# Optimization experiments

Measured on AMD Instinct MI355X. Metric: run time of the kernel, lower is better.

## Reference

```python
import jax, jax.numpy as jnp
import numpy as np

IN_FEATURES = 4096
OUT_FEATURES = 11008
GROUP_SIZE = 128
N_HIGH = 1024   # int(0.25*4096)//8*8
N_LOW = 3072    # (4096-1024)//8*8
M_TOKENS = 64


def unpack_6bit(packed, original_k):
    # packed: [K*3//4, N] uint8 values stored as int32
    _, N = packed.shape
    p = packed.reshape(original_k // 4, 3, N)
    b0, b1, b2 = p[:, 0], p[:, 1], p[:, 2]
    v0 = b0 & 63
    v1 = ((b0 >> 6) & 3) | ((b1 & 15) << 2)
    v2 = ((b1 >> 4) & 15) | ((b2 & 3) << 4)
    v3 = (b2 >> 2) & 63
    return jnp.stack([v0, v1, v2, v3], axis=1).reshape(original_k, N)


def unpack_5bit(packed, original_k):
    # packed: [K*5//8, N]
    _, N = packed.shape
    p = packed.reshape(original_k // 8, 5, N)
    b = [p[:, i] for i in range(5)]
    v0 = b[0] & 31
    v1 = ((b[0] >> 5) & 7) | ((b[1] & 3) << 3)
    v2 = (b[1] >> 2) & 31
    v3 = ((b[1] >> 7) & 1) | ((b[2] & 15) << 1)
    v4 = ((b[2] >> 4) & 15) | ((b[3] & 1) << 4)
    v5 = (b[3] >> 1) & 31
    v6 = ((b[3] >> 6) & 3) | ((b[4] & 7) << 2)
    v7 = (b[4] >> 3) & 31
    return jnp.stack([v0, v1, v2, v3, v4, v5, v6, v7], axis=1).reshape(original_k, N)


def dequant_region(W_q, scales, half_range):
    # W_q: [K, N] ints in [0, 2*half_range]; scales: [num_groups, N]
    K, N = W_q.shape
    G = scales.shape[0]
    Wg = (W_q.astype(jnp.float32) - float(half_range)).reshape(G, GROUP_SIZE, N)
    return (Wg * scales[:, None, :]).reshape(K, N)


def setup_inputs() -> dict:
    key = jax.random.key(0)
    ks = jax.random.split(key, 7)
    x = jax.random.normal(ks[0], (M_TOKENS, IN_FEATURES), dtype=jnp.float32)
    W_high_packed = jax.random.randint(ks[1], (N_HIGH * 3 // 4, OUT_FEATURES), 0, 256, dtype=jnp.int32)
    W_low_packed = jax.random.randint(ks[2], (N_LOW * 5 // 8, OUT_FEATURES), 0, 256, dtype=jnp.int32)
    scales_high = jax.random.uniform(ks[3], (N_HIGH // GROUP_SIZE, OUT_FEATURES), dtype=jnp.float32) * 0.02 + 1e-4
    scales_low = jax.random.uniform(ks[4], (N_LOW // GROUP_SIZE, OUT_FEATURES), dtype=jnp.float32) * 0.02 + 1e-4
    col_indices = jax.random.permutation(ks[5], IN_FEATURES).astype(jnp.int32)
    bias = jax.random.normal(ks[6], (OUT_FEATURES,), dtype=jnp.float32) * 0.02
    return {"x": x, "W_high_packed": W_high_packed, "W_low_packed": W_low_packed,
            "scales_high": scales_high, "scales_low": scales_low,
            "col_indices": col_indices, "bias": bias}


def reference(x, W_high_packed, W_low_packed, scales_high, scales_low, col_indices, bias):
    # Unpack mixed 6-bit / 5-bit weights and group-dequantize.
    Wq_high = unpack_6bit(W_high_packed, N_HIGH)          # [1024, N], 0..63
    Wq_low = unpack_5bit(W_low_packed, N_LOW)             # [3072, N], 0..31
    W_high = dequant_region(Wq_high, scales_high, 31)     # 6-bit half_range = 31
    W_low = dequant_region(Wq_low, scales_low, 15)        # 5-bit half_range = 15
    # Column-sensitivity reorder of activations, then split high/low regions.
    x_perm = x[:, col_indices]                            # [M, K]
    x_high = x_perm[:, :N_HIGH]
    x_low = x_perm[:, N_HIGH:N_HIGH + N_LOW]
    out = x_high @ W_high + x_low @ W_low + bias          # [M, N]
    return out
```

## Files before the change

kernel.cpp:

```cpp
#include <hip/hip_runtime.h>


#define NFEAT 11008
#define KTOT  4096

typedef _Float16 half8 __attribute__((ext_vector_type(8)));
typedef float    f32x4 __attribute__((ext_vector_type(4)));

__global__ __launch_bounds__(256) void prep_xfrag(const float* __restrict__ x,
                                                  const int* __restrict__ col,
                                                  _Float16* __restrict__ xfrag) {
    int idx = blockIdx.x * 256 + threadIdx.x;
    int j  = idx & 7;
    int l  = (idx >> 3) & 63;
    int mt = (idx >> 9) & 3;
    int s  = idx >> 11;
    int k  = s * 32 + ((l >> 4) << 3) + j;
    int m  = mt * 16 + (l & 15);
    xfrag[idx] = (_Float16)x[m * KTOT + col[k]];
}

__global__ __launch_bounds__(256, 4) void gemm_kernel(const int* __restrict__ Wh,
                                                      const int* __restrict__ Wl,
                                                      const float* __restrict__ sh,
                                                      const float* __restrict__ sl,
                                                      const _Float16* __restrict__ xfrag,
                                                      float* __restrict__ dst,
                                                      int atomic_mode) {
    const int n0   = blockIdx.x * 64;
    const int kc   = blockIdx.y;
    const int klen = KTOT / gridDim.y;
    const int k0   = kc * klen;
    const int lane = threadIdx.x & 63;
    const int wave = threadIdx.x >> 6;

    const int n  = n0 + wave * 16 + (lane & 15);
    const int kb = (lane >> 4) << 3;

    f32x4 acc[4];
#pragma unroll
    for (int i = 0; i < 4; ++i) acc[i] = (f32x4){0.f, 0.f, 0.f, 0.f};

    const int ngroups = klen >> 7;

    if (k0 < 1024) {
        for (int g = 0; g < ngroups; ++g) {
            const float s    = sh[((k0 >> 7) + g) * NFEAT + n];
            const float moff = -31.0f * s;
#pragma unroll
            for (int st = 0; st < 4; ++st) {
                const int k = k0 + g * 128 + st * 32 + kb;
                const int G = k >> 2;
                const int* bp = Wh + 3 * G * NFEAT + n;
                const int b0 = bp[0];         const int b1 = bp[NFEAT];
                const int b2 = bp[2 * NFEAT]; const int b3 = bp[3 * NFEAT];
                const int b4 = bp[4 * NFEAT]; const int b5 = bp[5 * NFEAT];
                int v0 = b0 & 63;
                int v1 = ((b0 >> 6) & 3) | ((b1 & 15) << 2);
                int v2 = ((b1 >> 4) & 15) | ((b2 & 3) << 4);
                int v3 = (b2 >> 2) & 63;
                int v4 = b3 & 63;
                int v5 = ((b3 >> 6) & 3) | ((b4 & 15) << 2);
                int v6 = ((b4 >> 4) & 15) | ((b5 & 3) << 4);
                int v7 = (b5 >> 2) & 63;
                half8 b;
                b[0] = (_Float16)fmaf((float)v0, s, moff);
                b[1] = (_Float16)fmaf((float)v1, s, moff);
                b[2] = (_Float16)fmaf((float)v2, s, moff);
                b[3] = (_Float16)fmaf((float)v3, s, moff);
                b[4] = (_Float16)fmaf((float)v4, s, moff);
                b[5] = (_Float16)fmaf((float)v5, s, moff);
                b[6] = (_Float16)fmaf((float)v6, s, moff);
                b[7] = (_Float16)fmaf((float)v7, s, moff);
                const int sg = (k0 >> 5) + g * 4 + st;
#pragma unroll
                for (int mt = 0; mt < 4; ++mt) {
                    half8 a = *(const half8*)(xfrag + (((sg * 4 + mt) * 64 + lane) << 3));
                    acc[mt] = __builtin_amdgcn_mfma_f32_16x16x32_f16(a, b, acc[mt], 0, 0, 0);
                }
            }
        }
    } else {
        const int kl0 = k0 - 1024;
        for (int g = 0; g < ngroups; ++g) {
            const float s    = sl[((kl0 >> 7) + g) * NFEAT + n];
            const float moff = -15.0f * s;
#pragma unroll
            for (int st = 0; st < 4; ++st) {
                const int kl = kl0 + g * 128 + st * 32 + kb;
                const int G8 = kl >> 3;
                const int* bp = Wl + 5 * G8 * NFEAT + n;
                const int b0 = bp[0];         const int b1 = bp[NFEAT];
                const int b2 = bp[2 * NFEAT]; const int b3 = bp[3 * NFEAT];
                const int b4 = bp[4 * NFEAT];
                int v0 = b0 & 31;
                int v1 = ((b0 >> 5) & 7) | ((b1 & 3) << 3);
                int v2 = (b1 >> 2) & 31;
                int v3 = ((b1 >> 7) & 1) | ((b2 & 15) << 1);
                int v4 = ((b2 >> 4) & 15) | ((b3 & 1) << 4);
                int v5 = (b3 >> 1) & 31;
                int v6 = ((b3 >> 6) & 3) | ((b4 & 7) << 2);
                int v7 = (b4 >> 3) & 31;
                half8 b;
                b[0] = (_Float16)fmaf((float)v0, s, moff);
                b[1] = (_Float16)fmaf((float)v1, s, moff);
                b[2] = (_Float16)fmaf((float)v2, s, moff);
                b[3] = (_Float16)fmaf((float)v3, s, moff);
                b[4] = (_Float16)fmaf((float)v4, s, moff);
                b[5] = (_Float16)fmaf((float)v5, s, moff);
                b[6] = (_Float16)fmaf((float)v6, s, moff);
                b[7] = (_Float16)fmaf((float)v7, s, moff);
                const int sg = 32 + (kl0 >> 5) + g * 4 + st;
#pragma unroll
                for (int mt = 0; mt < 4; ++mt) {
                    half8 a = *(const half8*)(xfrag + (((sg * 4 + mt) * 64 + lane) << 3));
                    acc[mt] = __builtin_amdgcn_mfma_f32_16x16x32_f16(a, b, acc[mt], 0, 0, 0);
                }
            }
        }
    }

    const int r0 = (lane >> 4) << 2;
    if (atomic_mode) {
#pragma unroll
        for (int mt = 0; mt < 4; ++mt)
#pragma unroll
            for (int r = 0; r < 4; ++r)
                atomicAdd(&dst[(mt * 16 + r0 + r) * NFEAT + n], acc[mt][r]);
    } else {
        float* base = dst + (size_t)kc * 64 * NFEAT;
#pragma unroll
        for (int mt = 0; mt < 4; ++mt)
#pragma unroll
            for (int r = 0; r < 4; ++r)
                base[(mt * 16 + r0 + r) * NFEAT + n] = acc[mt][r];
    }
}

__global__ __launch_bounds__(256) void reduce_out(const float* __restrict__ part,
                                                  const float* __restrict__ bias,
                                                  float* __restrict__ out, int nc) {
    const int idx = blockIdx.x * 256 + threadIdx.x;
    const int f   = idx * 4;
    const int n   = f % NFEAT;
    f32x4 sum = *(const f32x4*)(bias + n);
    for (int c = 0; c < nc; ++c)
        sum += *(const f32x4*)(part + (size_t)c * 704512 + f);
    *(f32x4*)(out + f) = sum;
}

__global__ __launch_bounds__(256) void init_bias(const float* __restrict__ bias,
                                                 float* __restrict__ out) {
    const int idx = blockIdx.x * 256 + threadIdx.x;
    out[idx] = bias[idx % NFEAT];
}

extern "C" void kernel_launch(void* const* d_in, const int* in_sizes, int n_in,
                              void* d_out, int out_size, void* d_ws, size_t ws_size,
                              hipStream_t stream) {
    const float* x    = (const float*)d_in[0];
    const int*   Wh   = (const int*)d_in[1];
    const int*   Wl   = (const int*)d_in[2];
    const float* sh   = (const float*)d_in[3];
    const float* sl   = (const float*)d_in[4];
    const int*   col  = (const int*)d_in[5];
    const float* bias = (const float*)d_in[6];
    float* out = (float*)d_out;

    _Float16* xfrag = (_Float16*)d_ws;
    const size_t xfrag_bytes = 64 * KTOT * sizeof(_Float16);
    const size_t part1 = 64ull * NFEAT * sizeof(float);

    prep_xfrag<<<1024, 256, 0, stream>>>(x, col, xfrag);

    if (ws_size >= xfrag_bytes + 8 * part1) {
        float* part = (float*)((char*)d_ws + xfrag_bytes);
        gemm_kernel<<<dim3(172, 8), 256, 0, stream>>>(Wh, Wl, sh, sl, xfrag, part, 0);
        reduce_out<<<688, 256, 0, stream>>>(part, bias, out, 8);
    } else if (ws_size >= xfrag_bytes + 4 * part1) {
        float* part = (float*)((char*)d_ws + xfrag_bytes);
        gemm_kernel<<<dim3(172, 4), 256, 0, stream>>>(Wh, Wl, sh, sl, xfrag, part, 0);
        reduce_out<<<688, 256, 0, stream>>>(part, bias, out, 4);
    } else {
        init_bias<<<2752, 256, 0, stream>>>(bias, out);
        gemm_kernel<<<dim3(172, 8), 256, 0, stream>>>(Wh, Wl, sh, sl, xfrag, out, 1);
    }
}
```

Before: 193.3 us.

## Stage packed weights and activations through LDS with async global-to-LDS pipeline

The GEMM now copies packed weight rows and activation fragments into a 4-slot shared-memory ring using global_load_lds. Each step prefetches two steps ahead, paced by vmcnt waits and barriers, so weight loads become coalesced row copies that overlap with dequant and MFMA work. The K split drops from 8 to 4 chunks, with chunk 0 covering the 6-bit region and chunks 1–3 the 5-bit region. Scales are preloaded into registers, and occupancy drops to 3 blocks per CU to make room for the LDS. Fewer blocks means less parallelism and more work per block, and the hand-counted waits could break if the compiler reorders loads.

Measured after the change: 173.0 us. 1.12x faster.

```diff
diff --git a/kernel.cpp b/kernel.cpp
--- a/kernel.cpp
+++ b/kernel.cpp
@@ -6,6 +6,14 @@
 
 typedef _Float16 half8 __attribute__((ext_vector_type(8)));
 typedef float    f32x4 __attribute__((ext_vector_type(4)));
+
+#define GLOAD4(g, l)  __builtin_amdgcn_global_load_lds(                         \
+    (const __attribute__((address_space(1))) unsigned int*)(g),                 \
+    (__attribute__((address_space(3))) unsigned int*)(l), 4, 0, 0)
+#define GLOAD16(g, l) __builtin_amdgcn_global_load_lds(                         \
+    (const __attribute__((address_space(1))) unsigned int*)(g),                 \
+    (__attribute__((address_space(3))) unsigned int*)(l), 16, 0, 0)
+#define WAITV(N) asm volatile("s_waitcnt vmcnt(" #N ")" ::: "memory")
 
 __global__ __launch_bounds__(256) void prep_xfrag(const float* __restrict__ x,
                                                   const int* __restrict__ col,
@@ -20,7 +28,7 @@
     xfrag[idx] = (_Float16)x[m * KTOT + col[k]];
 }
 
-__global__ __launch_bounds__(256, 4) void gemm_kernel(const int* __restrict__ Wh,
+__global__ __launch_bounds__(256, 3) void gemm_kernel(const int* __restrict__ Wh,
                                                       const int* __restrict__ Wl,
                                                       const float* __restrict__ sh,
                                                       const float* __restrict__ sl,
@@ -29,32 +37,54 @@
                                                       int atomic_mode) {
     const int n0   = blockIdx.x * 64;
     const int kc   = blockIdx.y;
-    const int klen = KTOT / gridDim.y;
-    const int k0   = kc * klen;
     const int lane = threadIdx.x & 63;
     const int wave = threadIdx.x >> 6;
-
-    const int n  = n0 + wave * 16 + (lane & 15);
-    const int kb = (lane >> 4) << 3;
+    const int cb   = wave * 16 + (lane & 15);
+    const int n    = n0 + cb;
+    const int o    = lane >> 4;
+
+    __shared__ int Wb[4][1632];
+    __shared__ __align__(16) _Float16 Ab[4][4][512];
 
     f32x4 acc[4];
 #pragma unroll
     for (int i = 0; i < 4; ++i) acc[i] = (f32x4){0.f, 0.f, 0.f, 0.f};
 
-    const int ngroups = klen >> 7;
-
-    if (k0 < 1024) {
-        for (int g = 0; g < ngroups; ++g) {
-            const float s    = sh[((k0 >> 7) + g) * NFEAT + n];
-            const float moff = -31.0f * s;
-#pragma unroll
+    if (kc == 0) {
+        float sc[8];
+#pragma unroll
+        for (int g = 0; g < 8; ++g) sc[g] = sh[g * NFEAT + n];
+
+#define STAGE6(T) do {                                                         \
+        const int _t = (T); const int _b = _t & 3;                             \
+        const int* _gs = Wh + (_t * 24 + wave * 6) * NFEAT + n0 + lane;        \
+        GLOAD4(_gs,             &Wb[_b][(wave * 6 + 0) * 68]);                 \
+        GLOAD4(_gs + 1 * NFEAT, &Wb[_b][(wave * 6 + 1) * 68]);                 \
+        GLOAD4(_gs + 2 * NFEAT, &Wb[_b][(wave * 6 + 2) * 68]);                 \
+        GLOAD4(_gs + 3 * NFEAT, &Wb[_b][(wave * 6 + 3) * 68]);                 \
+        GLOAD4(_gs + 4 * NFEAT, &Wb[_b][(wave * 6 + 4) * 68]);                 \
+        GLOAD4(_gs + 5 * NFEAT, &Wb[_b][(wave * 6 + 5) * 68]);                 \
+        GLOAD16(xfrag + ((size_t)(_t * 4 + wave) * 64 + lane) * 8,             \
+                &Ab[_b][wave][0]);                                             \
+    } while (0)
+
+        STAGE6(0);
+        STAGE6(1);
+#pragma unroll
+        for (int g = 0; g < 8; ++g) {
             for (int st = 0; st < 4; ++st) {
-                const int k = k0 + g * 128 + st * 32 + kb;
-                const int G = k >> 2;
-                const int* bp = Wh + 3 * G * NFEAT + n;
-                const int b0 = bp[0];         const int b1 = bp[NFEAT];
-                const int b2 = bp[2 * NFEAT]; const int b3 = bp[3 * NFEAT];
-                const int b4 = bp[4 * NFEAT]; const int b5 = bp[5 * NFEAT];
+                const int t = g * 4 + st;
+                if (t + 2 < 32) { STAGE6(t + 2); WAITV(14); }
+                else if (t + 1 < 32) { WAITV(7); }
+                else { WAITV(0); }
+                __builtin_amdgcn_s_barrier();
+                asm volatile("" ::: "memory");
+
+                const int  bi = t & 3;
+                const int* wr = &Wb[bi][(o * 6) * 68 + cb];
+                const int b0 = wr[0];      const int b1 = wr[68];
+                const int b2 = wr[2 * 68]; const int b3 = wr[3 * 68];
+                const int b4 = wr[4 * 68]; const int b5 = wr[5 * 68];
                 int v0 = b0 & 63;
                 int v1 = ((b0 >> 6) & 3) | ((b1 & 15) << 2);
                 int v2 = ((b1 >> 4) & 15) | ((b2 & 3) << 4);
@@ -63,36 +93,60 @@
                 int v5 = ((b3 >> 6) & 3) | ((b4 & 15) << 2);
                 int v6 = ((b4 >> 4) & 15) | ((b5 & 3) << 4);
                 int v7 = (b5 >> 2) & 63;
-                half8 b;
-                b[0] = (_Float16)fmaf((float)v0, s, moff);
-                b[1] = (_Float16)fmaf((float)v1, s, moff);
-                b[2] = (_Float16)fmaf((float)v2, s, moff);
-                b[3] = (_Float16)fmaf((float)v3, s, moff);
-                b[4] = (_Float16)fmaf((float)v4, s, moff);
-                b[5] = (_Float16)fmaf((float)v5, s, moff);
-                b[6] = (_Float16)fmaf((float)v6, s, moff);
-                b[7] = (_Float16)fmaf((float)v7, s, moff);
-                const int sg = (k0 >> 5) + g * 4 + st;
+                const float s = sc[g], moff = -31.0f * sc[g];
+                half8 bf;
+                bf[0] = (_Float16)fmaf((float)v0, s, moff);
+                bf[1] = (_Float16)fmaf((float)v1, s, moff);
+                bf[2] = (_Float16)fmaf((float)v2, s, moff);
+                bf[3] = (_Float16)fmaf((float)v3, s, moff);
+                bf[4] = (_Float16)fmaf((float)v4, s, moff);
+                bf[5] = (_Float16)fmaf((float)v5, s, moff);
+                bf[6] = (_Float16)fmaf((float)v6, s, moff);
+                bf[7] = (_Float16)fmaf((float)v7, s, moff);
 #pragma unroll
                 for (int mt = 0; mt < 4; ++mt) {
-                    half8 a = *(const half8*)(xfrag + (((sg * 4 + mt) * 64 + lane) << 3));
-                    acc[mt] = __builtin_amdgcn_mfma_f32_16x16x32_f16(a, b, acc[mt], 0, 0, 0);
+                    half8 a = *(const half8*)&Ab[bi][mt][lane * 8];
+                    acc[mt] = __builtin_amdgcn_mfma_f32_16x16x32_f16(a, bf, acc[mt], 0, 0, 0);
                 }
             }
         }
+#undef STAGE6
     } else {
-        const int kl0 = k0 - 1024;
-        for (int g = 0; g < ngroups; ++g) {
-            const float s    = sl[((kl0 >> 7) + g) * NFEAT + n];
-            const float moff = -15.0f * s;
-#pragma unroll
+        const int klc   = kc - 1;
+        const int rbase = klc * 640;
+        float sc[8];
+#pragma unroll
+        for (int g = 0; g < 8; ++g) sc[g] = sl[(klc * 8 + g) * NFEAT + n];
+
+#define STAGE5(T) do {                                                         \
+        const int _t = (T); const int _b = _t & 3;                             \
+        const int* _gs = Wl + (rbase + _t * 20 + wave * 5) * NFEAT + n0 + lane;\
+        GLOAD4(_gs,             &Wb[_b][(wave * 5 + 0) * 72]);                 \
+        GLOAD4(_gs + 1 * NFEAT, &Wb[_b][(wave * 5 + 1) * 72]);                 \
+        GLOAD4(_gs + 2 * NFEAT, &Wb[_b][(wave * 5 + 2) * 72]);                 \
+        GLOAD4(_gs + 3 * NFEAT, &Wb[_b][(wave * 5 + 3) * 72]);                 \
+        GLOAD4(_gs + 4 * NFEAT, &Wb[_b][(wave * 5 + 4) * 72]);                 \
+        GLOAD16(xfrag + ((size_t)((kc * 32 + _t) * 4 + wave) * 64 + lane) * 8, \
+                &Ab[_b][wave][0]);                                             \
+    } while (0)
+
+        STAGE5(0);
+        STAGE5(1);
+#pragma unroll
+        for (int g = 0; g < 8; ++g) {
             for (int st = 0; st < 4; ++st) {
-                const int kl = kl0 + g * 128 + st * 32 + kb;
-                const int G8 = kl >> 3;
-                const int* bp = Wl + 5 * G8 * NFEAT + n;
-                const int b0 = bp[0];         const int b1 = bp[NFEAT];
-                const int b2 = bp[2 * NFEAT]; const int b3 = bp[3 * NFEAT];
-                const int b4 = bp[4 * NFEAT];
+                const int t = g * 4 + st;
+                if (t + 2 < 32) { STAGE5(t + 2); WAITV(12); }
+                else if (t + 1 < 32) { WAITV(6); }
+                else { WAITV(0); }
+                __builtin_amdgcn_s_barrier();
+                asm volatile("" ::: "memory");
+
+                const int  bi = t & 3;
+                const int* wr = &Wb[bi][(o * 5) * 72 + cb];
+                const int b0 = wr[0];      const int b1 = wr[72];
+                const int b2 = wr[2 * 72]; const int b3 = wr[3 * 72];
+                const int b4 = wr[4 * 72];
                 int v0 = b0 & 31;
                 int v1 = ((b0 >> 5) & 7) | ((b1 & 3) << 3);
                 int v2 = (b1 >> 2) & 31;
@@ -101,23 +155,24 @@
                 int v5 = (b3 >> 1) & 31;
                 int v6 = ((b3 >> 6) & 3) | ((b4 & 7) << 2);
                 int v7 = (b4 >> 3) & 31;
-                half8 b;
-                b[0] = (_Float16)fmaf((float)v0, s, moff);
-                b[1] = (_Float16)fmaf((float)v1, s, moff);
-                b[2] = (_Float16)fmaf((float)v2, s, moff);
-                b[3] = (_Float16)fmaf((float)v3, s, moff);
-                b[4] = (_Float16)fmaf((float)v4, s, moff);
-                b[5] = (_Float16)fmaf((float)v5, s, moff);
-                b[6] = (_Float16)fmaf((float)v6, s, moff);
-                b[7] = (_Float16)fmaf((float)v7, s, moff);
-                const int sg = 32 + (kl0 >> 5) + g * 4 + st;
+                const float s = sc[g], moff = -15.0f * sc[g];
+                half8 bf;
+                bf[0] = (_Float16)fmaf((float)v0, s, moff);
+                bf[1] = (_Float16)fmaf((float)v1, s, moff);
+                bf[2] = (_Float16)fmaf((float)v2, s, moff);
+                bf[3] = (_Float16)fmaf((float)v3, s, moff);
+                bf[4] = (_Float16)fmaf((float)v4, s, moff);
+                bf[5] = (_Float16)fmaf((float)v5, s, moff);
+                bf[6] = (_Float16)fmaf((float)v6, s, moff);
+                bf[7] = (_Float16)fmaf((float)v7, s, moff);
 #pragma unroll
                 for (int mt = 0; mt < 4; ++mt) {
-                    half8 a = *(const half8*)(xfrag + (((sg * 4 + mt) * 64 + lane) << 3));
-                    acc[mt] = __builtin_amdgcn_mfma_f32_16x16x32_f16(a, b, acc[mt], 0, 0, 0);
+                    half8 a = *(const half8*)&Ab[bi][mt][lane * 8];
+                    acc[mt] = __builtin_amdgcn_mfma_f32_16x16x32_f16(a, bf, acc[mt], 0, 0, 0);
                 }
             }
         }
+#undef STAGE5
     }
 
     const int r0 = (lane >> 4) << 2;
@@ -173,16 +228,13 @@
 
     prep_xfrag<<<1024, 256, 0, stream>>>(x, col, xfrag);
 
-    if (ws_size >= xfrag_bytes + 8 * part1) {
+    dim3 grid(172, 4);
+    if (ws_size >= xfrag_bytes + 4 * part1) {
         float* part = (float*)((char*)d_ws + xfrag_bytes);
-        gemm_kernel<<<dim3(172, 8), 256, 0, stream>>>(Wh, Wl, sh, sl, xfrag, part, 0);
-        reduce_out<<<688, 256, 0, stream>>>(part, bias, out, 8);
-    } else if (ws_size >= xfrag_bytes + 4 * part1) {
-        float* part = (float*)((char*)d_ws + xfrag_bytes);
-        gemm_kernel<<<dim3(172, 4), 256, 0, stream>>>(Wh, Wl, sh, sl, xfrag, part, 0);
+        gemm_kernel<<<grid, 256, 0, stream>>>(Wh, Wl, sh, sl, xfrag, part, 0);
         reduce_out<<<688, 256, 0, stream>>>(part, bias, out, 4);
     } else {
         init_bias<<<2752, 256, 0, stream>>>(bias, out);
-        gemm_kernel<<<dim3(172, 8), 256, 0, stream>>>(Wh, Wl, sh, sl, xfrag, out, 1);
+        gemm_kernel<<<grid, 256, 0, stream>>>(Wh, Wl, sh, sl, xfrag, out, 1);
     }
 }
```

## Compact int32 weights to bytes per call and stream through LDS pipeline

Applied to the files above, without the earlier changes.

Adds a per-call pre-pass that narrows each int32-stored packed weight byte to a real byte, written into a swizzled per-tile layout in workspace. The GEMM then loads these compact tiles and the activation fragments into LDS with async global_load_lds in a three-buffer pipeline. It also widens each block to 128 output columns and stages the scales in LDS. The compaction pass still reads the full int32 weight array and adds a write, so the GEMM's traffic cut must outweigh an extra kernel launch and extra memory passes.

New measurement: 189.9 us. No clear change (-1.8%).

```diff
diff --git a/kernel.cpp b/kernel.cpp
--- a/kernel.cpp
+++ b/kernel.cpp
@@ -4,8 +4,20 @@
 #define NFEAT 11008
 #define KTOT  4096
 
+#define HTILE 98304u
+#define LTILE 245760u
+#define LBASE 8454144u
+#define CSIZE 29589504u
+
 typedef _Float16 half8 __attribute__((ext_vector_type(8)));
 typedef float    f32x4 __attribute__((ext_vector_type(4)));
+typedef int      int2v __attribute__((ext_vector_type(2)));
+
+#define GLOAD16(g, l) __builtin_amdgcn_global_load_lds(                         \
+    (const __attribute__((address_space(1))) unsigned int*)(g),                 \
+    (__attribute__((address_space(3))) unsigned int*)(l), 16, 0, 0)
+#define WAITV(N) asm volatile("s_waitcnt vmcnt(" #N ")" ::: "memory")
+#define FENCE()  asm volatile("" ::: "memory")
 
 __global__ __launch_bounds__(256) void prep_xfrag(const float* __restrict__ x,
                                                   const int* __restrict__ col,
@@ -20,20 +32,203 @@
     xfrag[idx] = (_Float16)x[m * KTOT + col[k]];
 }
 
-__global__ __launch_bounds__(256, 4) void gemm_kernel(const int* __restrict__ Wh,
-                                                      const int* __restrict__ Wl,
+__global__ __launch_bounds__(256) void compact_w(const int* __restrict__ Wh,
+                                                 const int* __restrict__ Wl,
+                                                 unsigned char* __restrict__ C) {
+    const int bx  = blockIdx.x;
+    const int y   = blockIdx.y;
+    const int sub = threadIdx.x >> 6;
+    const int l2  = (threadIdx.x & 63) * 2;
+    const int*     src;
+    unsigned char* dst;
+    int r;
+    if (y < 192) {
+        r   = y * 4 + sub;
+        src = Wh + (size_t)r * NFEAT + bx * 128;
+        dst = C + (size_t)bx * HTILE + r * 128;
+    } else {
+        r   = (y - 192) * 4 + sub;
+        src = Wl + (size_t)r * NFEAT + bx * 128;
+        dst = C + LBASE + (size_t)bx * LTILE + r * 128;
+    }
+    int2v v = *(const int2v*)(src + l2);
+    unsigned short p = (unsigned short)((v.x & 255) | ((v.y & 255) << 8));
+    const int pos = (l2 + ((r & 7) << 4)) & 127;
+    *(unsigned short*)(dst + pos) = p;
+}
+
+__global__ __launch_bounds__(256, 3) void gemm_kernel(const unsigned char* __restrict__ C,
                                                       const float* __restrict__ sh,
                                                       const float* __restrict__ sl,
                                                       const _Float16* __restrict__ xfrag,
                                                       float* __restrict__ dst,
                                                       int atomic_mode) {
+    const int bx   = blockIdx.x;
+    const int kc   = blockIdx.y;
+    const int lane = threadIdx.x & 63;
+    const int wave = threadIdx.x >> 6;
+    const int n0   = bx * 128;
+    const int o    = lane >> 4;
+    const int cc   = wave * 32 + (lane & 15);
+
+    __shared__ __align__(16) unsigned char Wb[3][6144];
+    __shared__ __align__(16) _Float16 Ab[3][8][512];
+    __shared__ float sLds[4][128];
+
+    const bool high = (kc < 2);
+
+    {
+        const float* sp = high ? sh + (size_t)(kc * 4) * NFEAT
+                               : sl + (size_t)((kc - 2) * 4) * NFEAT;
+        for (int i = threadIdx.x; i < 512; i += 256)
+            sLds[i >> 7][i & 127] = sp[(size_t)(i >> 7) * NFEAT + n0 + (i & 127)];
+    }
+
+    f32x4 acc[4][2];
+#pragma unroll
+    for (int i = 0; i < 4; ++i)
+#pragma unroll
+        for (int j = 0; j < 2; ++j) acc[i][j] = (f32x4){0.f, 0.f, 0.f, 0.f};
+
+    __syncthreads();
+
+    const unsigned char* cbase = high
+        ? C + (size_t)bx * HTILE + (size_t)kc * 49152
+        : C + LBASE + (size_t)bx * LTILE + (size_t)(kc - 2) * 40960;
+    const int stepb = high ? 6144 : 5120;
+
+    auto stage = [&](int t, int buf) {
+        const unsigned char* wsrc = cbase + (size_t)t * stepb;
+        GLOAD16(wsrc + wave * 1024 + lane * 16, &Wb[buf][wave * 1024]);
+        if (high) {
+            if (wave < 2) GLOAD16(wsrc + (wave + 4) * 1024 + lane * 16,
+                                  &Wb[buf][(wave + 4) * 1024]);
+        } else {
+            if (wave == 0) GLOAD16(wsrc + 4 * 1024 + lane * 16, &Wb[buf][4 * 1024]);
+        }
+        const int sgb = kc * 16 + t * 2;
+        GLOAD16(xfrag + ((size_t)(sgb * 4 + wave) * 64 + lane) * 8,
+                &Ab[buf][wave][0]);
+        GLOAD16(xfrag + ((size_t)((sgb + 1) * 4 + wave) * 64 + lane) * 8,
+                &Ab[buf][4 + wave][0]);
+    };
+
+    auto LB = [&](int bi, int R, int c) -> int {
+        return (int)Wb[bi][R * 128 + ((c + ((R & 7) << 4)) & 127)];
+    };
+
+    stage(0, 0);
+    stage(1, 1);
+
+    const bool cnt4 = high ? (wave < 2) : (wave == 0);
+    for (int t = 0; t < 8; ++t) {
+        if (t < 7) { if (cnt4) WAITV(4); else WAITV(3); }
+        else       { WAITV(0); }
+        __builtin_amdgcn_s_barrier();
+        FENCE();
+        if (t + 2 < 8) stage(t + 2, (t + 2) % 3);
+        const int bi = t % 3;
+
+#pragma unroll
+        for (int ss = 0; ss < 2; ++ss) {
+            const int g = (t * 2 + ss) >> 2;
+#pragma unroll
+            for (int nt = 0; nt < 2; ++nt) {
+                const int c = cc + nt * 16;
+                const float s = sLds[g][c];
+                half8 bf;
+                if (high) {
+                    const int rb = ss * 24 + 6 * o;
+                    const int b0 = LB(bi, rb + 0, c);
+                    const int b1 = LB(bi, rb + 1, c);
+                    const int b2 = LB(bi, rb + 2, c);
+                    const int b3 = LB(bi, rb + 3, c);
+                    const int b4 = LB(bi, rb + 4, c);
+                    const int b5 = LB(bi, rb + 5, c);
+                    const int v0 = b0 & 63;
+                    const int v1 = ((b0 >> 6) & 3) | ((b1 & 15) << 2);
+                    const int v2 = ((b1 >> 4) & 15) | ((b2 & 3) << 4);
+                    const int v3 = (b2 >> 2) & 63;
+                    const int v4 = b3 & 63;
+                    const int v5 = ((b3 >> 6) & 3) | ((b4 & 15) << 2);
+                    const int v6 = ((b4 >> 4) & 15) | ((b5 & 3) << 4);
+                    const int v7 = (b5 >> 2) & 63;
+                    const float moff = -31.0f * s;
+                    bf[0] = (_Float16)fmaf((float)v0, s, moff);
+                    bf[1] = (_Float16)fmaf((float)v1, s, moff);
+                    bf[2] = (_Float16)fmaf((float)v2, s, moff);
+                    bf[3] = (_Float16)fmaf((float)v3, s, moff);
+                    bf[4] = (_Float16)fmaf((float)v4, s, moff);
+                    bf[5] = (_Float16)fmaf((float)v5, s, moff);
+                    bf[6] = (_Float16)fmaf((float)v6, s, moff);
+                    bf[7] = (_Float16)fmaf((float)v7, s, moff);
+                } else {
+                    const int rb = ss * 20 + 5 * o;
+                    const int b0 = LB(bi, rb + 0, c);
+                    const int b1 = LB(bi, rb + 1, c);
+                    const int b2 = LB(bi, rb + 2, c);
+                    const int b3 = LB(bi, rb + 3, c);
+                    const int b4 = LB(bi, rb + 4, c);
+                    const int v0 = b0 & 31;
+                    const int v1 = ((b0 >> 5) & 7) | ((b1 & 3) << 3);
+                    const int v2 = (b1 >> 2) & 31;
+                    const int v3 = ((b1 >> 7) & 1) | ((b2 & 15) << 1);
+                    const int v4 = ((b2 >> 4) & 15) | ((b3 & 1) << 4);
+                    const int v5 = (b3 >> 1) & 31;
+                    const int v6 = ((b3 >> 6) & 3) | ((b4 & 7) << 2);
+                    const int v7 = (b4 >> 3) & 31;
+                    const float moff = -15.0f * s;
+                    bf[0] = (_Float16)fmaf((float)v0, s, moff);
+                    bf[1] = (_Float16)fmaf((float)v1, s, moff);
+                    bf[2] = (_Float16)fmaf((float)v2, s, moff);
+                    bf[3] = (_Float16)fmaf((float)v3, s, moff);
+                    bf[4] = (_Float16)fmaf((float)v4, s, moff);
+                    bf[5] = (_Float16)fmaf((float)v5, s, moff);
+                    bf[6] = (_Float16)fmaf((float)v6, s, moff);
+                    bf[7] = (_Float16)fmaf((float)v7, s, moff);
+                }
+#pragma unroll
+                for (int mt = 0; mt < 4; ++mt) {
+                    half8 a = *(const half8*)&Ab[bi][ss * 4 + mt][lane * 8];
+                    acc[mt][nt] = __builtin_amdgcn_mfma_f32_16x16x32_f16(a, bf, acc[mt][nt], 0, 0, 0);
+                }
+            }
+        }
+    }
+
+    const int r0 = (lane >> 4) << 2;
+    if (atomic_mode) {
+#pragma unroll
+        for (int mt = 0; mt < 4; ++mt)
+#pragma unroll
+            for (int nt = 0; nt < 2; ++nt)
+#pragma unroll
+                for (int r = 0; r < 4; ++r)
+                    atomicAdd(&dst[(mt * 16 + r0 + r) * NFEAT + n0 + cc + nt * 16],
+                              acc[mt][nt][r]);
+    } else {
+        float* base = dst + (size_t)kc * 64 * NFEAT;
+#pragma unroll
+        for (int mt = 0; mt < 4; ++mt)
+#pragma unroll
+            for (int nt = 0; nt < 2; ++nt)
+#pragma unroll
+                for (int r = 0; r < 4; ++r)
+                    base[(mt * 16 + r0 + r) * NFEAT + n0 + cc + nt * 16] = acc[mt][nt][r];
+    }
+}
+
+__global__ __launch_bounds__(256, 4) void gemm_direct(const int* __restrict__ Wh,
+                                                      const int* __restrict__ Wl,
+                                                      const float* __restrict__ sh,
+                                                      const float* __restrict__ sl,
+                                                      const _Float16* __restrict__ xfrag,
+                                                      float* __restrict__ dst) {
     const int n0   = blockIdx.x * 64;
     const int kc   = blockIdx.y;
-    const int klen = KTOT / gridDim.y;
-    const int k0   = kc * klen;
+    const int k0   = kc * 512;
     const int lane = threadIdx.x & 63;
     const int wave = threadIdx.x >> 6;
-
     const int n  = n0 + wave * 16 + (lane & 15);
     const int kb = (lane >> 4) << 3;
 
@@ -41,17 +236,14 @@
 #pragma unroll
     for (int i = 0; i < 4; ++i) acc[i] = (f32x4){0.f, 0.f, 0.f, 0.f};
 
-    const int ngroups = klen >> 7;
-
     if (k0 < 1024) {
-        for (int g = 0; g < ngroups; ++g) {
+        for (int g = 0; g < 4; ++g) {
             const float s    = sh[((k0 >> 7) + g) * NFEAT + n];
             const float moff = -31.0f * s;
 #pragma unroll
             for (int st = 0; st < 4; ++st) {
                 const int k = k0 + g * 128 + st * 32 + kb;
-                const int G = k >> 2;
-                const int* bp = Wh + 3 * G * NFEAT + n;
+                const int* bp = Wh + 3 * (k >> 2) * NFEAT + n;
                 const int b0 = bp[0];         const int b1 = bp[NFEAT];
                 const int b2 = bp[2 * NFEAT]; const int b3 = bp[3 * NFEAT];
                 const int b4 = bp[4 * NFEAT]; const int b5 = bp[5 * NFEAT];
@@ -82,14 +274,13 @@
         }
     } else {
         const int kl0 = k0 - 1024;
-        for (int g = 0; g < ngroups; ++g) {
+        for (int g = 0; g < 4; ++g) {
             const float s    = sl[((kl0 >> 7) + g) * NFEAT + n];
             const float moff = -15.0f * s;
 #pragma unroll
             for (int st = 0; st < 4; ++st) {
                 const int kl = kl0 + g * 128 + st * 32 + kb;
-                const int G8 = kl >> 3;
-                const int* bp = Wl + 5 * G8 * NFEAT + n;
+                const int* bp = Wl + 5 * (kl >> 3) * NFEAT + n;
                 const int b0 = bp[0];         const int b1 = bp[NFEAT];
                 const int b2 = bp[2 * NFEAT]; const int b3 = bp[3 * NFEAT];
                 const int b4 = bp[4 * NFEAT];
@@ -121,20 +312,11 @@
     }
 
     const int r0 = (lane >> 4) << 2;
-    if (atomic_mode) {
-#pragma unroll
-        for (int mt = 0; mt < 4; ++mt)
-#pragma unroll
-            for (int r = 0; r < 4; ++r)
-                atomicAdd(&dst[(mt * 16 + r0 + r) * NFEAT + n], acc[mt][r]);
-    } else {
-        float* base = dst + (size_t)kc * 64 * NFEAT;
-#pragma unroll
-        for (int mt = 0; mt < 4; ++mt)
-#pragma unroll
-            for (int r = 0; r < 4; ++r)
-                base[(mt * 16 + r0 + r) * NFEAT + n] = acc[mt][r];
-    }
+#pragma unroll
+    for (int mt = 0; mt < 4; ++mt)
+#pragma unroll
+        for (int r = 0; r < 4; ++r)
+            atomicAdd(&dst[(mt * 16 + r0 + r) * NFEAT + n], acc[mt][r]);
 }
 
 __global__ __launch_bounds__(256) void reduce_out(const float* __restrict__ part,
@@ -168,21 +350,24 @@
     float* out = (float*)d_out;
 
     _Float16* xfrag = (_Float16*)d_ws;
-    const size_t xfrag_bytes = 64 * KTOT * sizeof(_Float16);
-    const size_t part1 = 64ull * NFEAT * sizeof(float);
+    const size_t xo = 524288;
+    const size_t part_bytes = 8ull * 64 * NFEAT * sizeof(float);
 
     prep_xfrag<<<1024, 256, 0, stream>>>(x, col, xfrag);
 
-    if (ws_size >= xfrag_bytes + 8 * part1) {
-        float* part = (float*)((char*)d_ws + xfrag_bytes);
-        gemm_kernel<<<dim3(172, 8), 256, 0, stream>>>(Wh, Wl, sh, sl, xfrag, part, 0);
+    if (ws_size >= xo + part_bytes + CSIZE) {
+        float*         part = (float*)((char*)d_ws + xo);
+        unsigned char* C    = (unsigned char*)d_ws + xo + part_bytes;
+        compact_w<<<dim3(86, 672), 256, 0, stream>>>(Wh, Wl, C);
+        gemm_kernel<<<dim3(86, 8), 256, 0, stream>>>(C, sh, sl, xfrag, part, 0);
         reduce_out<<<688, 256, 0, stream>>>(part, bias, out, 8);
-    } else if (ws_size >= xfrag_bytes + 4 * part1) {
-        float* part = (float*)((char*)d_ws + xfrag_bytes);
-        gemm_kernel<<<dim3(172, 4), 256, 0, stream>>>(Wh, Wl, sh, sl, xfrag, part, 0);
-        reduce_out<<<688, 256, 0, stream>>>(part, bias, out, 4);
+    } else if (ws_size >= xo + CSIZE) {
+        unsigned char* C = (unsigned char*)d_ws + xo;
+        compact_w<<<dim3(86, 672), 256, 0, stream>>>(Wh, Wl, C);
+        init_bias<<<2752, 256, 0, stream>>>(bias, out);
+        gemm_kernel<<<dim3(86, 8), 256, 0, stream>>>(C, sh, sl, xfrag, out, 1);
     } else {
         init_bias<<<2752, 256, 0, stream>>>(bias, out);
-        gemm_kernel<<<dim3(172, 8), 256, 0, stream>>>(Wh, Wl, sh, sl, xfrag, out, 1);
-    }
-}
+        gemm_direct<<<dim3(172, 8), 256, 0, stream>>>(Wh, Wl, sh, sl, xfrag, out);
+    }
+}
```

## Pre-unpack packed weights into MFMA-ordered byte layout and tile GEMM via LDS

Applied to the files above, without the earlier changes.

Adds a compact_w kernel that reads the int32-stored packed 6/5-bit weights, unpacks them to one byte per value and writes them in the per-lane MFMA fragment order, so the GEMM reads 8 contiguous bytes per lane instead of 5-6 strided int32 loads. The GEMM now handles 128 output columns per block, stages the activation fragments in LDS with global_load_lds, and preloads scales. This pass runs on every call, so it adds a full read of the int32 weights plus a write and re-read of a 45MB buffer, but the GEMM's own weight traffic and unpack ALU work drop. Whether it pays off depends on that extra pass costing less than the savings.

Measured after the change: 203.6 us. +5.3%, slower.

```diff
diff --git a/kernel.cpp b/kernel.cpp
--- a/kernel.cpp
+++ b/kernel.cpp
@@ -4,8 +4,27 @@
 #define NFEAT 11008
 #define KTOT  4096
 
-typedef _Float16 half8 __attribute__((ext_vector_type(8)));
-typedef float    f32x4 __attribute__((ext_vector_type(4)));
+#define C2SIZE 45088768u
+
+typedef _Float16     half8 __attribute__((ext_vector_type(8)));
+typedef float        f32x4 __attribute__((ext_vector_type(4)));
+typedef unsigned int u32x2 __attribute__((ext_vector_type(2)));
+typedef unsigned int u32x4 __attribute__((ext_vector_type(4)));
+
+#define GLOAD16(g, l) __builtin_amdgcn_global_load_lds(                         \
+    (const __attribute__((address_space(1))) unsigned int*)(g),                 \
+    (__attribute__((address_space(3))) unsigned int*)(l), 16, 0, 0)
+
+#define DEQ8(w, s, mo, bf) do {                                                 \
+    bf[0] = (_Float16)fmaf((float)((w)[0]         & 255u), (s), (mo));          \
+    bf[1] = (_Float16)fmaf((float)(((w)[0] >>  8) & 255u), (s), (mo));          \
+    bf[2] = (_Float16)fmaf((float)(((w)[0] >> 16) & 255u), (s), (mo));          \
+    bf[3] = (_Float16)fmaf((float)( (w)[0] >> 24        ), (s), (mo));          \
+    bf[4] = (_Float16)fmaf((float)((w)[1]         & 255u), (s), (mo));          \
+    bf[5] = (_Float16)fmaf((float)(((w)[1] >>  8) & 255u), (s), (mo));          \
+    bf[6] = (_Float16)fmaf((float)(((w)[1] >> 16) & 255u), (s), (mo));          \
+    bf[7] = (_Float16)fmaf((float)( (w)[1] >> 24        ), (s), (mo));          \
+} while (0)
 
 __global__ __launch_bounds__(256) void prep_xfrag(const float* __restrict__ x,
                                                   const int* __restrict__ col,
@@ -20,20 +39,166 @@
     xfrag[idx] = (_Float16)x[m * KTOT + col[k]];
 }
 
-__global__ __launch_bounds__(256, 4) void gemm_kernel(const int* __restrict__ Wh,
-                                                      const int* __restrict__ Wl,
+__global__ __launch_bounds__(256) void compact_w(const int* __restrict__ Wh,
+                                                 const int* __restrict__ Wl,
+                                                 unsigned char* __restrict__ C2) {
+    const int bx  = blockIdx.x;
+    const int y   = blockIdx.y;
+    const int tid = threadIdx.x;
+    __shared__ unsigned char Lb[24][132];
+
+    const bool high = (y < 32);
+    const int  s    = high ? y : y - 32;
+    const int  nrow = high ? 24 : 20;
+    const int* src  = (high ? Wh + (size_t)(24 * s) * NFEAT
+                            : Wl + (size_t)(20 * s) * NFEAT) + bx * 128;
+    const int nint = nrow * 128;
+    for (int i = tid; i < nint; i += 256)
+        Lb[i >> 7][i & 127] = (unsigned char)(src[(size_t)(i >> 7) * NFEAT + (i & 127)] & 255);
+    __syncthreads();
+
+    const int sg  = high ? s : 32 + s;
+    const int L   = (2 * tid) & 63;
+    const int gcl = tid >> 5;
+    const int o   = L >> 4;
+
+    unsigned int ow[4];
+#pragma unroll
+    for (int u = 0; u < 2; ++u) {
+        const int c = gcl * 16 + ((L + u) & 15);
+        unsigned int v0, v1, v2, v3, v4, v5, v6, v7;
+        if (high) {
+            const unsigned int b0 = Lb[6 * o + 0][c], b1 = Lb[6 * o + 1][c];
+            const unsigned int b2 = Lb[6 * o + 2][c], b3 = Lb[6 * o + 3][c];
+            const unsigned int b4 = Lb[6 * o + 4][c], b5 = Lb[6 * o + 5][c];
+            v0 = b0 & 63;
+            v1 = ((b0 >> 6) & 3) | ((b1 & 15) << 2);
+            v2 = ((b1 >> 4) & 15) | ((b2 & 3) << 4);
+            v3 = (b2 >> 2) & 63;
+            v4 = b3 & 63;
+            v5 = ((b3 >> 6) & 3) | ((b4 & 15) << 2);
+            v6 = ((b4 >> 4) & 15) | ((b5 & 3) << 4);
+            v7 = (b5 >> 2) & 63;
+        } else {
+            const unsigned int b0 = Lb[5 * o + 0][c], b1 = Lb[5 * o + 1][c];
+            const unsigned int b2 = Lb[5 * o + 2][c], b3 = Lb[5 * o + 3][c];
+            const unsigned int b4 = Lb[5 * o + 4][c];
+            v0 = b0 & 31;
+            v1 = ((b0 >> 5) & 7) | ((b1 & 3) << 3);
+            v2 = (b1 >> 2) & 31;
+            v3 = ((b1 >> 7) & 1) | ((b2 & 15) << 1);
+            v4 = ((b2 >> 4) & 15) | ((b3 & 1) << 4);
+            v5 = (b3 >> 1) & 31;
+            v6 = ((b3 >> 6) & 3) | ((b4 & 7) << 2);
+            v7 = (b4 >> 3) & 31;
+        }
+        ow[2 * u]     = v0 | (v1 << 8) | (v2 << 16) | (v3 << 24);
+        ow[2 * u + 1] = v4 | (v5 << 8) | (v6 << 16) | (v7 << 24);
+    }
+    const size_t gc = (size_t)bx * 8 + gcl;
+    u32x4* dp = (u32x4*)(C2 + (gc * 128 + sg) * 512 + L * 8);
+    *dp = (u32x4){ow[0], ow[1], ow[2], ow[3]};
+}
+
+__global__ __launch_bounds__(256, 2) void gemm_kernel(const unsigned char* __restrict__ C2,
                                                       const float* __restrict__ sh,
                                                       const float* __restrict__ sl,
                                                       const _Float16* __restrict__ xfrag,
                                                       float* __restrict__ dst,
                                                       int atomic_mode) {
+    const int bx   = blockIdx.x;
+    const int kc   = blockIdx.y;
+    const int lane = threadIdx.x & 63;
+    const int wave = threadIdx.x >> 6;
+    const int ci   = lane & 15;
+    const int n0   = bx * 128;
+
+    __shared__ __align__(16) _Float16 Ald[32768];
+
+    {
+        const char* asrc = (const char*)xfrag + (size_t)kc * 65536;
+        const char* ldst = (char*)Ald;
+#pragma unroll
+        for (int i = 0; i < 16; ++i)
+            GLOAD16(asrc + ((size_t)threadIdx.x + i * 256) * 16,
+                    ldst + ((size_t)threadIdx.x + i * 256) * 16);
+    }
+
+    const bool  high = (kc < 2);
+    const float hr   = high ? 31.0f : 15.0f;
+    float sc[4][2], mo[4][2];
+#pragma unroll
+    for (int g = 0; g < 4; ++g)
+#pragma unroll
+        for (int ng = 0; ng < 2; ++ng) {
+            const int n = n0 + wave * 32 + ng * 16 + ci;
+            const float s = high ? sh[(size_t)(kc * 4 + g) * NFEAT + n]
+                                 : sl[(size_t)((kc - 2) * 4 + g) * NFEAT + n];
+            sc[g][ng] = s;
+            mo[g][ng] = -hr * s;
+        }
+
+    const size_t gc0 = (size_t)bx * 8 + wave * 2;
+    const unsigned char* bW0 = C2 + ((gc0 + 0) * 128 + kc * 16) * 512 + lane * 8;
+    const unsigned char* bW1 = C2 + ((gc0 + 1) * 128 + kc * 16) * 512 + lane * 8;
+
+    f32x4 acc[4][2];
+#pragma unroll
+    for (int i = 0; i < 4; ++i)
+#pragma unroll
+        for (int j = 0; j < 2; ++j) acc[i][j] = (f32x4){0.f, 0.f, 0.f, 0.f};
+
+    __syncthreads();
+
+#pragma unroll
+    for (int t = 0; t < 16; ++t) {
+        const u32x2 w0 = *(const u32x2*)(bW0 + t * 512);
+        const u32x2 w1 = *(const u32x2*)(bW1 + t * 512);
+        const int g = t >> 2;
+        half8 b0, b1;
+        DEQ8(w0, sc[g][0], mo[g][0], b0);
+        DEQ8(w1, sc[g][1], mo[g][1], b1);
+#pragma unroll
+        for (int mt = 0; mt < 4; ++mt) {
+            half8 a = *(const half8*)&Ald[((t * 4 + mt) * 64 + lane) * 8];
+            acc[mt][0] = __builtin_amdgcn_mfma_f32_16x16x32_f16(a, b0, acc[mt][0], 0, 0, 0);
+            acc[mt][1] = __builtin_amdgcn_mfma_f32_16x16x32_f16(a, b1, acc[mt][1], 0, 0, 0);
+        }
+    }
+
+    const int r0 = (lane >> 4) << 2;
+    if (atomic_mode) {
+#pragma unroll
+        for (int mt = 0; mt < 4; ++mt)
+#pragma unroll
+            for (int ng = 0; ng < 2; ++ng)
+#pragma unroll
+                for (int r = 0; r < 4; ++r)
+                    atomicAdd(&dst[(size_t)(mt * 16 + r0 + r) * NFEAT + n0 + wave * 32 + ng * 16 + ci],
+                              acc[mt][ng][r]);
+    } else {
+        float* base = dst + (size_t)kc * 64 * NFEAT;
+#pragma unroll
+        for (int mt = 0; mt < 4; ++mt)
+#pragma unroll
+            for (int ng = 0; ng < 2; ++ng)
+#pragma unroll
+                for (int r = 0; r < 4; ++r)
+                    base[(size_t)(mt * 16 + r0 + r) * NFEAT + n0 + wave * 32 + ng * 16 + ci] = acc[mt][ng][r];
+    }
+}
+
+__global__ __launch_bounds__(256, 4) void gemm_direct(const int* __restrict__ Wh,
+                                                      const int* __restrict__ Wl,
+                                                      const float* __restrict__ sh,
+                                                      const float* __restrict__ sl,
+                                                      const _Float16* __restrict__ xfrag,
+                                                      float* __restrict__ dst) {
     const int n0   = blockIdx.x * 64;
     const int kc   = blockIdx.y;
-    const int klen = KTOT / gridDim.y;
-    const int k0   = kc * klen;
+    const int k0   = kc * 512;
     const int lane = threadIdx.x & 63;
     const int wave = threadIdx.x >> 6;
-
     const int n  = n0 + wave * 16 + (lane & 15);
     const int kb = (lane >> 4) << 3;
 
@@ -41,17 +206,14 @@
 #pragma unroll
     for (int i = 0; i < 4; ++i) acc[i] = (f32x4){0.f, 0.f, 0.f, 0.f};
 
-    const int ngroups = klen >> 7;
-
     if (k0 < 1024) {
-        for (int g = 0; g < ngroups; ++g) {
+        for (int g = 0; g < 4; ++g) {
             const float s    = sh[((k0 >> 7) + g) * NFEAT + n];
             const float moff = -31.0f * s;
 #pragma unroll
             for (int st = 0; st < 4; ++st) {
                 const int k = k0 + g * 128 + st * 32 + kb;
-                const int G = k >> 2;
-                const int* bp = Wh + 3 * G * NFEAT + n;
+                const int* bp = Wh + 3 * (k >> 2) * NFEAT + n;
                 const int b0 = bp[0];         const int b1 = bp[NFEAT];
                 const int b2 = bp[2 * NFEAT]; const int b3 = bp[3 * NFEAT];
                 const int b4 = bp[4 * NFEAT]; const int b5 = bp[5 * NFEAT];
@@ -82,14 +244,13 @@
         }
     } else {
         const int kl0 = k0 - 1024;
-        for (int g = 0; g < ngroups; ++g) {
+        for (int g = 0; g < 4; ++g) {
             const float s    = sl[((kl0 >> 7) + g) * NFEAT + n];
             const float moff = -15.0f * s;
 #pragma unroll
             for (int st = 0; st < 4; ++st) {
                 const int kl = kl0 + g * 128 + st * 32 + kb;
-                const int G8 = kl >> 3;
-                const int* bp = Wl + 5 * G8 * NFEAT + n;
+                const int* bp = Wl + 5 * (kl >> 3) * NFEAT + n;
                 const int b0 = bp[0];         const int b1 = bp[NFEAT];
                 const int b2 = bp[2 * NFEAT]; const int b3 = bp[3 * NFEAT];
                 const int b4 = bp[4 * NFEAT];
@@ -121,20 +282,11 @@
     }
 
     const int r0 = (lane >> 4) << 2;
-    if (atomic_mode) {
-#pragma unroll
-        for (int mt = 0; mt < 4; ++mt)
-#pragma unroll
-            for (int r = 0; r < 4; ++r)
-                atomicAdd(&dst[(mt * 16 + r0 + r) * NFEAT + n], acc[mt][r]);
-    } else {
-        float* base = dst + (size_t)kc * 64 * NFEAT;
-#pragma unroll
-        for (int mt = 0; mt < 4; ++mt)
-#pragma unroll
-            for (int r = 0; r < 4; ++r)
-                base[(mt * 16 + r0 + r) * NFEAT + n] = acc[mt][r];
-    }
+#pragma unroll
+    for (int mt = 0; mt < 4; ++mt)
+#pragma unroll
+        for (int r = 0; r < 4; ++r)
+            atomicAdd(&dst[(mt * 16 + r0 + r) * NFEAT + n], acc[mt][r]);
 }
 
 __global__ __launch_bounds__(256) void reduce_out(const float* __restrict__ part,
@@ -168,21 +320,24 @@
     float* out = (float*)d_out;
 
     _Float16* xfrag = (_Float16*)d_ws;
-    const size_t xfrag_bytes = 64 * KTOT * sizeof(_Float16);
-    const size_t part1 = 64ull * NFEAT * sizeof(float);
+    const size_t xo = 524288;
+    const size_t part_bytes = 8ull * 64 * NFEAT * sizeof(float);
 
     prep_xfrag<<<1024, 256, 0, stream>>>(x, col, xfrag);
 
-    if (ws_size >= xfrag_bytes + 8 * part1) {
-        float* part = (float*)((char*)d_ws + xfrag_bytes);
-        gemm_kernel<<<dim3(172, 8), 256, 0, stream>>>(Wh, Wl, sh, sl, xfrag, part, 0);
+    if (ws_size >= xo + part_bytes + C2SIZE) {
+        float*         part = (float*)((char*)d_ws + xo);
+        unsigned char* C2   = (unsigned char*)d_ws + xo + part_bytes;
+        compact_w<<<dim3(86, 128), 256, 0, stream>>>(Wh, Wl, C2);
+        gemm_kernel<<<dim3(86, 8), 256, 0, stream>>>(C2, sh, sl, xfrag, part, 0);
         reduce_out<<<688, 256, 0, stream>>>(part, bias, out, 8);
-    } else if (ws_size >= xfrag_bytes + 4 * part1) {
-        float* part = (float*)((char*)d_ws + xfrag_bytes);
-        gemm_kernel<<<dim3(172, 4), 256, 0, stream>>>(Wh, Wl, sh, sl, xfrag, part, 0);
-        reduce_out<<<688, 256, 0, stream>>>(part, bias, out, 4);
+    } else if (ws_size >= xo + C2SIZE) {
+        unsigned char* C2 = (unsigned char*)d_ws + xo;
+        compact_w<<<dim3(86, 128), 256, 0, stream>>>(Wh, Wl, C2);
+        init_bias<<<2752, 256, 0, stream>>>(bias, out);
+        gemm_kernel<<<dim3(86, 8), 256, 0, stream>>>(C2, sh, sl, xfrag, out, 1);
     } else {
         init_bias<<<2752, 256, 0, stream>>>(bias, out);
-        gemm_kernel<<<dim3(172, 8), 256, 0, stream>>>(Wh, Wl, sh, sl, xfrag, out, 1);
-    }
-}
+        gemm_direct<<<dim3(172, 8), 256, 0, stream>>>(Wh, Wl, sh, sl, xfrag, out);
+    }
+}
```
